# Optimization experiments

Measured on AMD Instinct MI355X. Metric: run time of the kernel, lower is better.

## Reference

```python
import jax, jax.numpy as jnp
import numpy as np

NUM_HEADS = 32
HEAD_DIM = 128
NUM_KV_HEADS = 8
SCALE = 1.0 / np.sqrt(HEAD_DIM)
BATCH = 8
SEQ = 1024
TOTAL = BATCH * SEQ


def setup_inputs() -> dict:
    key = jax.random.key(0)
    kq, kk, kv = jax.random.split(key, 3)
    q = jax.random.normal(kq, (TOTAL, NUM_HEADS * HEAD_DIM), dtype=jnp.float32)
    k = jax.random.normal(kk, (TOTAL, NUM_KV_HEADS * HEAD_DIM), dtype=jnp.float32)
    v = jax.random.normal(kv, (TOTAL, NUM_KV_HEADS * HEAD_DIM), dtype=jnp.float32)
    cu = (jnp.arange(BATCH + 1, dtype=jnp.int32) * SEQ)
    return {"q": q, "k": k, "v": v, "cu_seqlens_q": cu, "cu_seqlens_k": cu}


def reference(q, k, v, cu_seqlens_q, cu_seqlens_k):
    # Prefill path of Attention.forward: causal varlen GQA flash attention.
    # Equal-length sequences -> reshape flat tokens into [B, S, ...].
    B = cu_seqlens_q.shape[0] - 1          # static: number of sequences
    T = q.shape[0]
    S = T // B
    G = NUM_HEADS // NUM_KV_HEADS          # query heads per kv head
    qr = q.reshape(B, S, NUM_KV_HEADS, G, HEAD_DIM)
    kr = k.reshape(B, S, NUM_KV_HEADS, HEAD_DIM)
    vr = v.reshape(B, S, NUM_KV_HEADS, HEAD_DIM)
    # scores: [B, Hkv, G, Sq, Sk]
    scores = jnp.einsum('bqhgd,bkhd->bhgqk', qr, kr) * jnp.float32(SCALE)
    causal = jnp.tril(jnp.ones((S, S), dtype=bool))  # [Sq, Sk]
    scores = jnp.where(causal, scores, jnp.finfo(scores.dtype).min)
    probs = jax.nn.softmax(scores, axis=-1)
    o = jnp.einsum('bhgqk,bkhd->bqhgd', probs, vr)
    return o.reshape(T, NUM_HEADS * HEAD_DIM)
```

## Files before the change

kernel.cpp:

```cpp
#include <hip/hip_runtime.h>
#include <hip/hip_bf16.h>
#include <stdint.h>

typedef __bf16 bf16_t;
typedef __attribute__((ext_vector_type(8))) __bf16 bf16x8;
typedef __attribute__((ext_vector_type(4))) __bf16 bf16x4;
typedef __attribute__((ext_vector_type(4))) float f32x4;

#define NHEADS 32
#define HDIM 128
#define NKV 8
#define GQ 4
#define BATCH 8
#define SEQ 1024
#define TOTAL (BATCH * SEQ)
#define QD (NHEADS * HDIM)
#define KVD (NKV * HDIM)
#define ATT_SCALE 0.08838834764831845f
#define QSCL (0.08838834764831845f * 1.4426950408889634f)

#define QBLK 64
#define KBLK 64
#define NQT (SEQ / QBLK)

__device__ __forceinline__ void gload16(const bf16_t* g, bf16_t* l) {
    __builtin_amdgcn_global_load_lds(
        (const __attribute__((address_space(1))) void*)g,
        (__attribute__((address_space(3))) void*)l,
        16, 0, 0);
}

__global__ __launch_bounds__(256)
void attn_prepass_kernel(const float* __restrict__ kg, const float* __restrict__ vg,
                         bf16_t* __restrict__ kws, bf16_t* __restrict__ vtws)
{
    const int bid = blockIdx.x;
    const int tid = threadIdx.x;
    if (bid < 512) {
        __shared__ bf16_t Lt[128 * 130];
        const int b  = bid >> 6;
        const int hk = (bid >> 3) & 7;
        const int tt = bid & 7;
        const float* vp = vg + ((long)(b * SEQ + tt * 128)) * KVD + hk * HDIM;
        #pragma unroll
        for (int it = 0; it < 16; ++it) {
            int idx = it * 256 + tid;
            int t  = idx >> 5;
            int c4 = (idx & 31) * 4;
            float4 f = *(const float4*)(vp + (long)t * KVD + c4);
            Lt[(c4 + 0) * 130 + t] = (bf16_t)f.x;
            Lt[(c4 + 1) * 130 + t] = (bf16_t)f.y;
            Lt[(c4 + 2) * 130 + t] = (bf16_t)f.z;
            Lt[(c4 + 3) * 130 + t] = (bf16_t)f.w;
        }
        __syncthreads();
        bf16_t* op = vtws + ((long)((b * NKV + hk) * HDIM)) * SEQ + tt * 128;
        #pragma unroll
        for (int jt = 0; jt < 8; ++jt) {
            int jdx = jt * 256 + tid;
            int d  = jdx >> 4;
            int c8 = (jdx & 15) * 8;
            const bf16_t* lp = &Lt[d * 130 + c8];
            uint32_t u0 = *(const uint32_t*)(lp + 0);
            uint32_t u1 = *(const uint32_t*)(lp + 2);
            uint32_t u2 = *(const uint32_t*)(lp + 4);
            uint32_t u3 = *(const uint32_t*)(lp + 6);
            uint4 o; o.x = u0; o.y = u1; o.z = u2; o.w = u3;
            *(uint4*)(op + (long)d * SEQ + c8) = o;
        }
    } else {
        const long total4 = (long)TOTAL * KVD / 4;
        const float4* k4 = (const float4*)kg;
        for (long i = (long)(bid - 512) * 256 + tid; i < total4; i += 1024L * 256) {
            float4 f = k4[i];
            bf16x4 o4;
            o4[0] = (bf16_t)f.x; o4[1] = (bf16_t)f.y;
            o4[2] = (bf16_t)f.z; o4[3] = (bf16_t)f.w;
            *(bf16x4*)(kws + i * 4) = o4;
        }
    }
}

__global__ __launch_bounds__(512, 2)
void attn_fwd_v4(const float* __restrict__ qg, const bf16_t* __restrict__ kws,
                 const bf16_t* __restrict__ vtws, float* __restrict__ og)
{
    __shared__ __align__(16) bf16_t Kl[2][KBLK * HDIM];
    __shared__ __align__(16) bf16_t Vl[2][HDIM * KBLK];
    __shared__ __align__(16) bf16_t Pl[8][16 * 64];

    const int tid  = threadIdx.x;
    const int w    = tid >> 6;
    const int lane = tid & 63;
    const int l4   = lane >> 4;
    const int l16  = lane & 15;

    const int bid = blockIdx.x;
    const int bh  = bid & 63;
    const int pi  = bid >> 6;
    const int b   = bh >> 3;
    const int hk  = bh & 7;
    const int g   = w >> 1;
    const int h   = hk * GQ + g;
    const int rh  = (w & 1) * 32;

    const bf16_t* kbase = kws + (long)(b * SEQ) * KVD + hk * HDIM;
    const bf16_t* vbase = vtws + (long)((b * NKV + hk) * HDIM) * SEQ;
    const int kc0 = w * 2;

    auto issue_tile = [&](int buf, int kt) {
        #pragma unroll
        for (int i = 0; i < 2; ++i) {
            int c = kc0 + i;
            int r = c * 4 + (lane >> 4);
            const bf16_t* gp = kbase + (long)(kt * KBLK + r) * KVD + (((lane & 15) ^ (r & 7)) * 8);
            gload16(gp, &Kl[buf][c * 512]);
        }
        #pragma unroll
        for (int i = 0; i < 2; ++i) {
            int c = kc0 + i;
            int d = c * 8 + (lane >> 3);
            const bf16_t* gp = vbase + (long)d * SEQ + kt * KBLK + (((lane & 7) ^ (d & 7)) * 8);
            gload16(gp, &Vl[buf][c * 512]);
        }
    };

    for (int ph = 0; ph < 2; ++ph) {
        const int qt = ph ? pi : (NQT - 1 - pi);
        const long qtok0 = (long)b * SEQ + qt * QBLK;

        bf16x8 aq[2][4];
        #pragma unroll
        for (int f = 0; f < 2; ++f) {
            const float* qp = qg + (qtok0 + rh + f * 16 + l16) * QD + h * HDIM + l4 * 8;
            #pragma unroll
            for (int s = 0; s < 4; ++s) {
                float4 x = *(const float4*)(qp + s * 32);
                float4 y = *(const float4*)(qp + s * 32 + 4);
                bf16x8 t;
                t[0] = (bf16_t)(x.x * QSCL); t[1] = (bf16_t)(x.y * QSCL);
                t[2] = (bf16_t)(x.z * QSCL); t[3] = (bf16_t)(x.w * QSCL);
                t[4] = (bf16_t)(y.x * QSCL); t[5] = (bf16_t)(y.y * QSCL);
                t[6] = (bf16_t)(y.z * QSCL); t[7] = (bf16_t)(y.w * QSCL);
                aq[f][s] = t;
            }
        }
        __builtin_amdgcn_sched_barrier(0);

        f32x4 accO[2][8];
        f32x4 rsum[2];
        #pragma unroll
        for (int f = 0; f < 2; ++f) {
            #pragma unroll
            for (int n = 0; n < 8; ++n) accO[f][n] = (f32x4){0.f, 0.f, 0.f, 0.f};
            rsum[f] = (f32x4){0.f, 0.f, 0.f, 0.f};
        }

        const int nkt = qt + 1;
        issue_tile(0, 0);
        if (nkt > 1) issue_tile(1, 1);

        for (int kt = 0; kt < nkt; ++kt) {
            const int cur = kt & 1;
            if (kt + 1 < nkt) asm volatile("s_waitcnt vmcnt(4)" ::: "memory");
            else              asm volatile("s_waitcnt vmcnt(0)" ::: "memory");
            __builtin_amdgcn_s_barrier();
            __builtin_amdgcn_sched_barrier(0);

            const bool diag = (kt == qt);
            bf16_t* pw = &Pl[w][0];
            const bf16_t* Kc = &Kl[cur][0];
            const bf16_t* Vc = &Vl[cur][0];

            #pragma unroll
            for (int f = 0; f < 2; ++f) {
                f32x4 accS[4];
                __builtin_amdgcn_s_setprio(1);
                #pragma unroll
                for (int n = 0; n < 4; ++n) {
                    f32x4 acc = (f32x4){0.f, 0.f, 0.f, 0.f};
                    const int r = n * 16 + l16;
                    #pragma unroll
                    for (int s = 0; s < 4; ++s) {
                        int cb = ((s * 64 + l4 * 16) ^ ((r & 7) << 4)) >> 1;
                        bf16x8 bk = *(const bf16x8*)(Kc + r * 128 + cb);
                        acc = __builtin_amdgcn_mfma_f32_16x16x32_bf16(aq[f][s], bk, acc, 0, 0, 0);
                    }
                    accS[n] = acc;
                }
                __builtin_amdgcn_s_setprio(0);

                const int qrow_loc = rh + f * 16 + l4 * 4;
                if (diag) {
                    #pragma unroll
                    for (int n = 0; n < 4; ++n) {
                        #pragma unroll
                        for (int j = 0; j < 4; ++j) {
                            float p = exp2f(accS[n][j]);
                            if (n * 16 + l16 > qrow_loc + j) p = 0.f;
                            accS[n][j] = p;
                            rsum[f][j] += p;
                        }
                    }
                } else {
                    #pragma unroll
                    for (int n = 0; n < 4; ++n) {
                        #pragma unroll
                        for (int j = 0; j < 4; ++j) {
                            float p = exp2f(accS[n][j]);
                            accS[n][j] = p;
                            rsum[f][j] += p;
                        }
                    }
                }

                #pragma unroll
                for (int n = 0; n < 4; ++n) {
                    #pragma unroll
                    for (int j = 0; j < 4; ++j) {
                        int qr = l4 * 4 + j;
                        int cbyte = (n * 32 + l16 * 2) ^ ((qr & 7) << 4);
                        pw[qr * 64 + (cbyte >> 1)] = (bf16_t)accS[n][j];
                    }
                }
                asm volatile("s_waitcnt lgkmcnt(0)" ::: "memory");
                __builtin_amdgcn_sched_barrier(0);
                __builtin_amdgcn_s_setprio(1);
                #pragma unroll
                for (int ks = 0; ks < 2; ++ks) {
                    int cbp = ((ks * 64 + l4 * 16) ^ ((l16 & 7) << 4)) >> 1;
                    bf16x8 ap = *(const bf16x8*)(pw + l16 * 64 + cbp);
                    #pragma unroll
                    for (int n = 0; n < 8; ++n) {
                        int d = n * 16 + l16;
                        int cb = ((ks * 64 + l4 * 16) ^ ((d & 7) << 4)) >> 1;
                        bf16x8 bv = *(const bf16x8*)(Vc + d * 64 + cb);
                        accO[f][n] = __builtin_amdgcn_mfma_f32_16x16x32_bf16(ap, bv, accO[f][n], 0, 0, 0);
                    }
                }
                __builtin_amdgcn_s_setprio(0);
            }
            __builtin_amdgcn_sched_barrier(0);
            __builtin_amdgcn_s_barrier();
            if (kt + 2 < nkt) issue_tile(cur, kt + 2);
        }

        #pragma unroll
        for (int f = 0; f < 2; ++f) {
            #pragma unroll
            for (int j = 0; j < 4; ++j) {
                float r = rsum[f][j];
                r += __shfl_xor(r, 1);
                r += __shfl_xor(r, 2);
                r += __shfl_xor(r, 4);
                r += __shfl_xor(r, 8);
                float inv = 1.f / r;
                float* op = og + (qtok0 + rh + f * 16 + l4 * 4 + j) * QD + h * HDIM;
                #pragma unroll
                for (int n = 0; n < 8; ++n)
                    op[n * 16 + l16] = accO[f][n][j] * inv;
            }
        }
    }
}

#define KPAD 136
#define VPAD 72
#define PPAD 72
__global__ __launch_bounds__(512, 2)
void attn_fwd_v1(const float* __restrict__ qg, const float* __restrict__ kg,
                 const float* __restrict__ vg, float* __restrict__ og)
{
    __shared__ bf16_t Kl[KBLK * KPAD];
    __shared__ bf16_t Vt[HDIM * VPAD];
    __shared__ bf16_t Pl[8 * 16 * PPAD];

    const int tid  = threadIdx.x;
    const int w    = tid >> 6;
    const int lane = tid & 63;
    const int l4   = lane >> 4;
    const int l16  = lane & 15;

    const int bid = blockIdx.x;
    const int bh  = bid % 64;
    const int qt  = (NQT - 1) - bid / 64;
    const int b   = bh / NKV;
    const int hk  = bh % NKV;
    const int g   = w >> 1;
    const int h   = hk * GQ + g;
    const int rh  = (w & 1) * 32;

    const long qtok0 = (long)b * SEQ + qt * QBLK;

    bf16x8 aq[2][4];
    #pragma unroll
    for (int f = 0; f < 2; ++f) {
        const float* qp = qg + (qtok0 + rh + f * 16 + l16) * QD + h * HDIM + l4 * 8;
        #pragma unroll
        for (int s = 0; s < 4; ++s) {
            float4 x = *(const float4*)(qp + s * 32);
            float4 y = *(const float4*)(qp + s * 32 + 4);
            bf16x8 t;
            t[0] = (bf16_t)x.x; t[1] = (bf16_t)x.y; t[2] = (bf16_t)x.z; t[3] = (bf16_t)x.w;
            t[4] = (bf16_t)y.x; t[5] = (bf16_t)y.y; t[6] = (bf16_t)y.z; t[7] = (bf16_t)y.w;
            aq[f][s] = t;
        }
    }

    f32x4 accO[2][8];
    float mrun[2][4], lsum[2][4];
    #pragma unroll
    for (int f = 0; f < 2; ++f) {
        #pragma unroll
        for (int n = 0; n < 8; ++n) accO[f][n] = (f32x4){0.f, 0.f, 0.f, 0.f};
        #pragma unroll
        for (int j = 0; j < 4; ++j) { mrun[f][j] = -1e30f; lsum[f][j] = 0.f; }
    }

    const long ktok0 = (long)b * SEQ;
    const int nkt = qt + 1;

    for (int kt = 0; kt < nkt; ++kt) {
        __syncthreads();
        const float* kp = kg + (ktok0 + kt * KBLK) * KVD + hk * HDIM;
        const float* vp = vg + (ktok0 + kt * KBLK) * KVD + hk * HDIM;
        #pragma unroll
        for (int it = 0; it < 4; ++it) {
            int idx = it * 512 + tid;
            int row = idx >> 5;
            int c4  = (idx & 31) * 4;
            float4 kf = *(const float4*)(kp + (long)row * KVD + c4);
            bf16x4 k4;
            k4[0] = (bf16_t)kf.x; k4[1] = (bf16_t)kf.y; k4[2] = (bf16_t)kf.z; k4[3] = (bf16_t)kf.w;
            *(bf16x4*)(&Kl[row * KPAD + c4]) = k4;
            float4 vf = *(const float4*)(vp + (long)row * KVD + c4);
            const float* vfa = (const float*)&vf;
            #pragma unroll
            for (int m = 0; m < 4; ++m) {
                int d   = c4 + m;
                int blk = (row >> 3) ^ ((d >> 3) & 7);
                Vt[d * VPAD + blk * 8 + (row & 7)] = (bf16_t)vfa[m];
            }
        }
        __syncthreads();

        const bool diag = (kt == qt);
        bf16_t* pw = &Pl[w * 16 * PPAD];

        #pragma unroll
        for (int f = 0; f < 2; ++f) {
            f32x4 accS[4];
            #pragma unroll
            for (int n = 0; n < 4; ++n) {
                f32x4 acc = (f32x4){0.f, 0.f, 0.f, 0.f};
                #pragma unroll
                for (int s = 0; s < 4; ++s) {
                    bf16x8 bk = *(const bf16x8*)(&Kl[(n * 16 + l16) * KPAD + s * 32 + l4 * 8]);
                    acc = __builtin_amdgcn_mfma_f32_16x16x32_bf16(aq[f][s], bk, acc, 0, 0, 0);
                }
                accS[n] = acc;
            }

            const int qrow_loc = rh + f * 16 + l4 * 4;
            float pm[4];
            #pragma unroll
            for (int j = 0; j < 4; ++j) pm[j] = -1e30f;
            #pragma unroll
            for (int n = 0; n < 4; ++n) {
                #pragma unroll
                for (int j = 0; j < 4; ++j) {
                    float sv = accS[n][j] * ATT_SCALE;
                    if (diag && (n * 16 + l16 > qrow_loc + j)) sv = -1e30f;
                    accS[n][j] = sv;
                    pm[j] = fmaxf(pm[j], sv);
                }
            }
            #pragma unroll
            for (int j = 0; j < 4; ++j) {
                float m0 = pm[j];
                m0 = fmaxf(m0, __shfl_xor(m0, 1));
                m0 = fmaxf(m0, __shfl_xor(m0, 2));
                m0 = fmaxf(m0, __shfl_xor(m0, 4));
                m0 = fmaxf(m0, __shfl_xor(m0, 8));
                pm[j] = m0;
            }
            float al[4], rs[4];
            #pragma unroll
            for (int j = 0; j < 4; ++j) {
                float mnew = fmaxf(mrun[f][j], pm[j]);
                al[j] = __expf(mrun[f][j] - mnew);
                mrun[f][j] = mnew;
                rs[j] = 0.f;
            }
            #pragma unroll
            for (int n = 0; n < 4; ++n) {
                #pragma unroll
                for (int j = 0; j < 4; ++j) {
                    float p = __expf(accS[n][j] - mrun[f][j]);
                    accS[n][j] = p;
                    rs[j] += p;
                }
            }
            #pragma unroll
            for (int j = 0; j < 4; ++j) {
                float r = rs[j];
                r += __shfl_xor(r, 1);
                r += __shfl_xor(r, 2);
                r += __shfl_xor(r, 4);
                r += __shfl_xor(r, 8);
                lsum[f][j] = lsum[f][j] * al[j] + r;
            }
            #pragma unroll
            for (int n = 0; n < 8; ++n) {
                #pragma unroll
                for (int j = 0; j < 4; ++j) accO[f][n][j] *= al[j];
            }
            #pragma unroll
            for (int n = 0; n < 4; ++n) {
                #pragma unroll
                for (int j = 0; j < 4; ++j)
                    pw[(l4 * 4 + j) * PPAD + n * 16 + l16] = (bf16_t)accS[n][j];
            }
            asm volatile("s_waitcnt lgkmcnt(0)" ::: "memory");
            __builtin_amdgcn_sched_barrier(0);
            #pragma unroll
            for (int ks = 0; ks < 2; ++ks) {
                bf16x8 ap = *(const bf16x8*)(&pw[l16 * PPAD + ks * 32 + l4 * 8]);
                #pragma unroll
                for (int n = 0; n < 8; ++n) {
                    int d   = n * 16 + l16;
                    int blk = (ks * 4 + l4) ^ ((d >> 3) & 7);
                    bf16x8 bv = *(const bf16x8*)(&Vt[d * VPAD + blk * 8]);
                    accO[f][n] = __builtin_amdgcn_mfma_f32_16x16x32_bf16(ap, bv, accO[f][n], 0, 0, 0);
                }
            }
        }
    }

    #pragma unroll
    for (int f = 0; f < 2; ++f) {
        #pragma unroll
        for (int j = 0; j < 4; ++j) {
            float inv = 1.f / lsum[f][j];
            float* op = og + (qtok0 + rh + f * 16 + l4 * 4 + j) * QD + h * HDIM;
            #pragma unroll
            for (int n = 0; n < 8; ++n)
                op[n * 16 + l16] = accO[f][n][j] * inv;
        }
    }
}

extern "C" void kernel_launch(void* const* d_in, const int* in_sizes, int n_in,
                              void* d_out, int out_size, void* d_ws, size_t ws_size,
                              hipStream_t stream) {
    const float* q = (const float*)d_in[0];
    const float* k = (const float*)d_in[1];
    const float* v = (const float*)d_in[2];
    float* o = (float*)d_out;

    const size_t kws_elems = (size_t)TOTAL * KVD;
    const size_t vws_elems = (size_t)BATCH * NKV * HDIM * SEQ;
    const size_t need = (kws_elems + vws_elems) * sizeof(bf16_t);

    if (ws_size >= need) {
        bf16_t* kws  = (bf16_t*)d_ws;
        bf16_t* vtws = kws + kws_elems;
        attn_prepass_kernel<<<1536, 256, 0, stream>>>(k, v, kws, vtws);
        attn_fwd_v4<<<512, 512, 0, stream>>>(q, kws, vtws, o);
    } else {
        attn_fwd_v1<<<NQT * BATCH * NKV, 512, 0, stream>>>(q, k, v, o);
    }
}
```

Before: 173.6 us.

## Split attention work across 16 waves per block, one 16-row strip each

Raises the attention block from 512 to 1024 threads so each of 16 waves handles one head and one 16-query-row strip instead of two strips. The aim is more waves in flight to hide latency, with fewer registers per wave and each wave loading a single K and V chunk per tile. In exchange the block barriers now synchronize twice as many waves, the P scratch buffer doubles, and launch bounds no longer request two blocks per CU.

```diff
diff --git a/kernel.cpp b/kernel.cpp
--- a/kernel.cpp
+++ b/kernel.cpp
@@ -81,13 +81,13 @@
     }
 }
 
-__global__ __launch_bounds__(512, 2)
-void attn_fwd_v4(const float* __restrict__ qg, const bf16_t* __restrict__ kws,
+__global__ __launch_bounds__(1024)
+void attn_fwd_v5(const float* __restrict__ qg, const bf16_t* __restrict__ kws,
                  const bf16_t* __restrict__ vtws, float* __restrict__ og)
 {
     __shared__ __align__(16) bf16_t Kl[2][KBLK * HDIM];
     __shared__ __align__(16) bf16_t Vl[2][HDIM * KBLK];
-    __shared__ __align__(16) bf16_t Pl[8][16 * 64];
+    __shared__ __align__(16) bf16_t Pl[16][16 * 64];
 
     const int tid  = threadIdx.x;
     const int w    = tid >> 6;
@@ -100,28 +100,23 @@
     const int pi  = bid >> 6;
     const int b   = bh >> 3;
     const int hk  = bh & 7;
-    const int g   = w >> 1;
+    const int g   = w >> 2;
+    const int fs  = w & 3;
     const int h   = hk * GQ + g;
-    const int rh  = (w & 1) * 32;
 
     const bf16_t* kbase = kws + (long)(b * SEQ) * KVD + hk * HDIM;
     const bf16_t* vbase = vtws + (long)((b * NKV + hk) * HDIM) * SEQ;
-    const int kc0 = w * 2;
 
     auto issue_tile = [&](int buf, int kt) {
-        #pragma unroll
-        for (int i = 0; i < 2; ++i) {
-            int c = kc0 + i;
-            int r = c * 4 + (lane >> 4);
+        {
+            int r = w * 4 + (lane >> 4);
             const bf16_t* gp = kbase + (long)(kt * KBLK + r) * KVD + (((lane & 15) ^ (r & 7)) * 8);
-            gload16(gp, &Kl[buf][c * 512]);
-        }
-        #pragma unroll
-        for (int i = 0; i < 2; ++i) {
-            int c = kc0 + i;
-            int d = c * 8 + (lane >> 3);
+            gload16(gp, &Kl[buf][w * 512]);
+        }
+        {
+            int d = w * 8 + (lane >> 3);
             const bf16_t* gp = vbase + (long)d * SEQ + kt * KBLK + (((lane & 7) ^ (d & 7)) * 8);
-            gload16(gp, &Vl[buf][c * 512]);
+            gload16(gp, &Vl[buf][w * 512]);
         }
     };
 
@@ -129,10 +124,9 @@
         const int qt = ph ? pi : (NQT - 1 - pi);
         const long qtok0 = (long)b * SEQ + qt * QBLK;
 
-        bf16x8 aq[2][4];
-        #pragma unroll
-        for (int f = 0; f < 2; ++f) {
-            const float* qp = qg + (qtok0 + rh + f * 16 + l16) * QD + h * HDIM + l4 * 8;
+        bf16x8 aq[4];
+        {
+            const float* qp = qg + (qtok0 + fs * 16 + l16) * QD + h * HDIM + l4 * 8;
             #pragma unroll
             for (int s = 0; s < 4; ++s) {
                 float4 x = *(const float4*)(qp + s * 32);
@@ -142,19 +136,16 @@
                 t[2] = (bf16_t)(x.z * QSCL); t[3] = (bf16_t)(x.w * QSCL);
                 t[4] = (bf16_t)(y.x * QSCL); t[5] = (bf16_t)(y.y * QSCL);
                 t[6] = (bf16_t)(y.z * QSCL); t[7] = (bf16_t)(y.w * QSCL);
-                aq[f][s] = t;
+                aq[s] = t;
             }
         }
         __builtin_amdgcn_sched_barrier(0);
 
-        f32x4 accO[2][8];
-        f32x4 rsum[2];
-        #pragma unroll
-        for (int f = 0; f < 2; ++f) {
-            #pragma unroll
-            for (int n = 0; n < 8; ++n) accO[f][n] = (f32x4){0.f, 0.f, 0.f, 0.f};
-            rsum[f] = (f32x4){0.f, 0.f, 0.f, 0.f};
-        }
+        f32x4 accO[8];
+        f32x4 rsum;
+        #pragma unroll
+        for (int n = 0; n < 8; ++n) accO[n] = (f32x4){0.f, 0.f, 0.f, 0.f};
+        rsum = (f32x4){0.f, 0.f, 0.f, 0.f};
 
         const int nkt = qt + 1;
         issue_tile(0, 0);
@@ -162,7 +153,7 @@
 
         for (int kt = 0; kt < nkt; ++kt) {
             const int cur = kt & 1;
-            if (kt + 1 < nkt) asm volatile("s_waitcnt vmcnt(4)" ::: "memory");
+            if (kt + 1 < nkt) asm volatile("s_waitcnt vmcnt(2)" ::: "memory");
             else              asm volatile("s_waitcnt vmcnt(0)" ::: "memory");
             __builtin_amdgcn_s_barrier();
             __builtin_amdgcn_sched_barrier(0);
@@ -172,94 +163,89 @@
             const bf16_t* Kc = &Kl[cur][0];
             const bf16_t* Vc = &Vl[cur][0];
 
-            #pragma unroll
-            for (int f = 0; f < 2; ++f) {
-                f32x4 accS[4];
-                __builtin_amdgcn_s_setprio(1);
-                #pragma unroll
-                for (int n = 0; n < 4; ++n) {
-                    f32x4 acc = (f32x4){0.f, 0.f, 0.f, 0.f};
-                    const int r = n * 16 + l16;
-                    #pragma unroll
-                    for (int s = 0; s < 4; ++s) {
-                        int cb = ((s * 64 + l4 * 16) ^ ((r & 7) << 4)) >> 1;
-                        bf16x8 bk = *(const bf16x8*)(Kc + r * 128 + cb);
-                        acc = __builtin_amdgcn_mfma_f32_16x16x32_bf16(aq[f][s], bk, acc, 0, 0, 0);
-                    }
-                    accS[n] = acc;
-                }
-                __builtin_amdgcn_s_setprio(0);
-
-                const int qrow_loc = rh + f * 16 + l4 * 4;
-                if (diag) {
-                    #pragma unroll
-                    for (int n = 0; n < 4; ++n) {
-                        #pragma unroll
-                        for (int j = 0; j < 4; ++j) {
-                            float p = exp2f(accS[n][j]);
-                            if (n * 16 + l16 > qrow_loc + j) p = 0.f;
-                            accS[n][j] = p;
-                            rsum[f][j] += p;
-                        }
-                    }
-                } else {
-                    #pragma unroll
-                    for (int n = 0; n < 4; ++n) {
-                        #pragma unroll
-                        for (int j = 0; j < 4; ++j) {
-                            float p = exp2f(accS[n][j]);
-                            accS[n][j] = p;
-                            rsum[f][j] += p;
-                        }
-                    }
-                }
-
+            f32x4 accS[4];
+            __builtin_amdgcn_s_setprio(1);
+            #pragma unroll
+            for (int n = 0; n < 4; ++n) {
+                f32x4 acc = (f32x4){0.f, 0.f, 0.f, 0.f};
+                const int r = n * 16 + l16;
+                #pragma unroll
+                for (int s = 0; s < 4; ++s) {
+                    int cb = ((s * 64 + l4 * 16) ^ ((r & 7) << 4)) >> 1;
+                    bf16x8 bk = *(const bf16x8*)(Kc + r * 128 + cb);
+                    acc = __builtin_amdgcn_mfma_f32_16x16x32_bf16(aq[s], bk, acc, 0, 0, 0);
+                }
+                accS[n] = acc;
+            }
+            __builtin_amdgcn_s_setprio(0);
+
+            const int qrow_loc = fs * 16 + l4 * 4;
+            if (diag) {
                 #pragma unroll
                 for (int n = 0; n < 4; ++n) {
                     #pragma unroll
                     for (int j = 0; j < 4; ++j) {
-                        int qr = l4 * 4 + j;
-                        int cbyte = (n * 32 + l16 * 2) ^ ((qr & 7) << 4);
-                        pw[qr * 64 + (cbyte >> 1)] = (bf16_t)accS[n][j];
+                        float p = exp2f(accS[n][j]);
+                        if (n * 16 + l16 > qrow_loc + j) p = 0.f;
+                        accS[n][j] = p;
+                        rsum[j] += p;
                     }
                 }
-                asm volatile("s_waitcnt lgkmcnt(0)" ::: "memory");
-                __builtin_amdgcn_sched_barrier(0);
-                __builtin_amdgcn_s_setprio(1);
-                #pragma unroll
-                for (int ks = 0; ks < 2; ++ks) {
-                    int cbp = ((ks * 64 + l4 * 16) ^ ((l16 & 7) << 4)) >> 1;
-                    bf16x8 ap = *(const bf16x8*)(pw + l16 * 64 + cbp);
+            } else {
+                #pragma unroll
+                for (int n = 0; n < 4; ++n) {
                     #pragma unroll
-                    for (int n = 0; n < 8; ++n) {
-                        int d = n * 16 + l16;
-                        int cb = ((ks * 64 + l4 * 16) ^ ((d & 7) << 4)) >> 1;
-                        bf16x8 bv = *(const bf16x8*)(Vc + d * 64 + cb);
-                        accO[f][n] = __builtin_amdgcn_mfma_f32_16x16x32_bf16(ap, bv, accO[f][n], 0, 0, 0);
+                    for (int j = 0; j < 4; ++j) {
+                        float p = exp2f(accS[n][j]);
+                        accS[n][j] = p;
+                        rsum[j] += p;
                     }
                 }
-                __builtin_amdgcn_s_setprio(0);
-            }
+            }
+
+            #pragma unroll
+            for (int n = 0; n < 4; ++n) {
+                #pragma unroll
+                for (int j = 0; j < 4; ++j) {
+                    int qr = l4 * 4 + j;
+                    int cbyte = (n * 32 + l16 * 2) ^ ((qr & 7) << 4);
+                    pw[qr * 64 + (cbyte >> 1)] = (bf16_t)accS[n][j];
+                }
+            }
+            asm volatile("s_waitcnt lgkmcnt(0)" ::: "memory");
+            __builtin_amdgcn_sched_barrier(0);
+            __builtin_amdgcn_s_setprio(1);
+            #pragma unroll
+            for (int ks = 0; ks < 2; ++ks) {
+                int cbp = ((ks * 64 + l4 * 16) ^ ((l16 & 7) << 4)) >> 1;
+                bf16x8 ap = *(const bf16x8*)(pw + l16 * 64 + cbp);
+                #pragma unroll
+                for (int n = 0; n < 8; ++n) {
+                    int d = n * 16 + l16;
+                    int cb = ((ks * 64 + l4 * 16) ^ ((d & 7) << 4)) >> 1;
+                    bf16x8 bv = *(const bf16x8*)(Vc + d * 64 + cb);
+                    accO[n] = __builtin_amdgcn_mfma_f32_16x16x32_bf16(ap, bv, accO[n], 0, 0, 0);
+                }
+            }
+            __builtin_amdgcn_s_setprio(0);
+
             __builtin_amdgcn_sched_barrier(0);
             __builtin_amdgcn_s_barrier();
             if (kt + 2 < nkt) issue_tile(cur, kt + 2);
         }
 
         #pragma unroll
-        for (int f = 0; f < 2; ++f) {
-            #pragma unroll
-            for (int j = 0; j < 4; ++j) {
-                float r = rsum[f][j];
-                r += __shfl_xor(r, 1);
-                r += __shfl_xor(r, 2);
-                r += __shfl_xor(r, 4);
-                r += __shfl_xor(r, 8);
-                float inv = 1.f / r;
-                float* op = og + (qtok0 + rh + f * 16 + l4 * 4 + j) * QD + h * HDIM;
-                #pragma unroll
-                for (int n = 0; n < 8; ++n)
-                    op[n * 16 + l16] = accO[f][n][j] * inv;
-            }
+        for (int j = 0; j < 4; ++j) {
+            float r = rsum[j];
+            r += __shfl_xor(r, 1);
+            r += __shfl_xor(r, 2);
+            r += __shfl_xor(r, 4);
+            r += __shfl_xor(r, 8);
+            float inv = 1.f / r;
+            float* op = og + (qtok0 + fs * 16 + l4 * 4 + j) * QD + h * HDIM;
+            #pragma unroll
+            for (int n = 0; n < 8; ++n)
+                op[n * 16 + l16] = accO[n][j] * inv;
         }
     }
 }
@@ -466,7 +452,7 @@
         bf16_t* kws  = (bf16_t*)d_ws;
         bf16_t* vtws = kws + kws_elems;
         attn_prepass_kernel<<<1536, 256, 0, stream>>>(k, v, kws, vtws);
-        attn_fwd_v4<<<512, 512, 0, stream>>>(q, kws, vtws, o);
+        attn_fwd_v5<<<512, 1024, 0, stream>>>(q, kws, vtws, o);
     } else {
         attn_fwd_v1<<<NQT * BATCH * NKV, 512, 0, stream>>>(q, k, v, o);
     }
```

Result: slower. 178.3 us (+2.7%).

## Switch attention inner loops to 32x32x16 MFMA tiles with diagonal-half skip

Applied to the files above, without the earlier changes.

Rewrites the per-wave QK^T and PV computation to use 32x32x16 bf16 MFMA instructions over a full 32-row query slice instead of two 16-row passes of 16x16x32 MFMAs. This cuts LDS operand reads per FLOP and the instruction count, and the P staging buffer grows to 32x64 per wave. On the diagonal tile, waves owning the upper 32 query rows skip the second key half entirely, since it is fully masked. The trade-off is larger accumulator register tiles (16 floats each), which may pressure registers at 2 blocks per CU.

```diff
diff --git a/kernel.cpp b/kernel.cpp
--- a/kernel.cpp
+++ b/kernel.cpp
@@ -6,6 +6,7 @@
 typedef __attribute__((ext_vector_type(8))) __bf16 bf16x8;
 typedef __attribute__((ext_vector_type(4))) __bf16 bf16x4;
 typedef __attribute__((ext_vector_type(4))) float f32x4;
+typedef __attribute__((ext_vector_type(16))) float f32x16;
 
 #define NHEADS 32
 #define HDIM 128
@@ -28,6 +29,13 @@
         (const __attribute__((address_space(1))) void*)g,
         (__attribute__((address_space(3))) void*)l,
         16, 0, 0);
+}
+
+__device__ __forceinline__ f32x16 zero16() {
+    f32x16 z;
+    #pragma unroll
+    for (int j = 0; j < 16; ++j) z[j] = 0.f;
+    return z;
 }
 
 __global__ __launch_bounds__(256)
@@ -82,18 +90,18 @@
 }
 
 __global__ __launch_bounds__(512, 2)
-void attn_fwd_v4(const float* __restrict__ qg, const bf16_t* __restrict__ kws,
+void attn_fwd_v6(const float* __restrict__ qg, const bf16_t* __restrict__ kws,
                  const bf16_t* __restrict__ vtws, float* __restrict__ og)
 {
     __shared__ __align__(16) bf16_t Kl[2][KBLK * HDIM];
     __shared__ __align__(16) bf16_t Vl[2][HDIM * KBLK];
-    __shared__ __align__(16) bf16_t Pl[8][16 * 64];
+    __shared__ __align__(16) bf16_t Pl[8][32 * 64];
 
     const int tid  = threadIdx.x;
     const int w    = tid >> 6;
     const int lane = tid & 63;
-    const int l4   = lane >> 4;
-    const int l16  = lane & 15;
+    const int l31  = lane & 31;
+    const int l2   = lane >> 5;
 
     const int bid = blockIdx.x;
     const int bh  = bid & 63;
@@ -101,8 +109,9 @@
     const int b   = bh >> 3;
     const int hk  = bh & 7;
     const int g   = w >> 1;
+    const int half = w & 1;
+    const int rh  = half * 32;
     const int h   = hk * GQ + g;
-    const int rh  = (w & 1) * 32;
 
     const bf16_t* kbase = kws + (long)(b * SEQ) * KVD + hk * HDIM;
     const bf16_t* vbase = vtws + (long)((b * NKV + hk) * HDIM) * SEQ;
@@ -129,32 +138,29 @@
         const int qt = ph ? pi : (NQT - 1 - pi);
         const long qtok0 = (long)b * SEQ + qt * QBLK;
 
-        bf16x8 aq[2][4];
-        #pragma unroll
-        for (int f = 0; f < 2; ++f) {
-            const float* qp = qg + (qtok0 + rh + f * 16 + l16) * QD + h * HDIM + l4 * 8;
-            #pragma unroll
-            for (int s = 0; s < 4; ++s) {
-                float4 x = *(const float4*)(qp + s * 32);
-                float4 y = *(const float4*)(qp + s * 32 + 4);
+        bf16x8 aq[8];
+        {
+            const float* qp = qg + (qtok0 + rh + l31) * QD + h * HDIM + l2 * 8;
+            #pragma unroll
+            for (int s = 0; s < 8; ++s) {
+                float4 x = *(const float4*)(qp + s * 16);
+                float4 y = *(const float4*)(qp + s * 16 + 4);
                 bf16x8 t;
                 t[0] = (bf16_t)(x.x * QSCL); t[1] = (bf16_t)(x.y * QSCL);
                 t[2] = (bf16_t)(x.z * QSCL); t[3] = (bf16_t)(x.w * QSCL);
                 t[4] = (bf16_t)(y.x * QSCL); t[5] = (bf16_t)(y.y * QSCL);
                 t[6] = (bf16_t)(y.z * QSCL); t[7] = (bf16_t)(y.w * QSCL);
-                aq[f][s] = t;
+                aq[s] = t;
             }
         }
         __builtin_amdgcn_sched_barrier(0);
 
-        f32x4 accO[2][8];
-        f32x4 rsum[2];
-        #pragma unroll
-        for (int f = 0; f < 2; ++f) {
-            #pragma unroll
-            for (int n = 0; n < 8; ++n) accO[f][n] = (f32x4){0.f, 0.f, 0.f, 0.f};
-            rsum[f] = (f32x4){0.f, 0.f, 0.f, 0.f};
-        }
+        f32x16 accO[4];
+        #pragma unroll
+        for (int n = 0; n < 4; ++n) accO[n] = zero16();
+        float rsum[16];
+        #pragma unroll
+        for (int r = 0; r < 16; ++r) rsum[r] = 0.f;
 
         const int nkt = qt + 1;
         issue_tile(0, 0);
@@ -167,99 +173,107 @@
             __builtin_amdgcn_s_barrier();
             __builtin_amdgcn_sched_barrier(0);
 
-            const bool diag = (kt == qt);
+            const bool diag  = (kt == qt);
+            const bool skip1 = diag && (rh == 0);
             bf16_t* pw = &Pl[w][0];
             const bf16_t* Kc = &Kl[cur][0];
             const bf16_t* Vc = &Vl[cur][0];
 
-            #pragma unroll
-            for (int f = 0; f < 2; ++f) {
-                f32x4 accS[4];
-                __builtin_amdgcn_s_setprio(1);
-                #pragma unroll
-                for (int n = 0; n < 4; ++n) {
-                    f32x4 acc = (f32x4){0.f, 0.f, 0.f, 0.f};
-                    const int r = n * 16 + l16;
-                    #pragma unroll
-                    for (int s = 0; s < 4; ++s) {
-                        int cb = ((s * 64 + l4 * 16) ^ ((r & 7) << 4)) >> 1;
-                        bf16x8 bk = *(const bf16x8*)(Kc + r * 128 + cb);
-                        acc = __builtin_amdgcn_mfma_f32_16x16x32_bf16(aq[f][s], bk, acc, 0, 0, 0);
-                    }
-                    accS[n] = acc;
-                }
-                __builtin_amdgcn_s_setprio(0);
-
-                const int qrow_loc = rh + f * 16 + l4 * 4;
-                if (diag) {
-                    #pragma unroll
-                    for (int n = 0; n < 4; ++n) {
-                        #pragma unroll
-                        for (int j = 0; j < 4; ++j) {
-                            float p = exp2f(accS[n][j]);
-                            if (n * 16 + l16 > qrow_loc + j) p = 0.f;
-                            accS[n][j] = p;
-                            rsum[f][j] += p;
-                        }
-                    }
-                } else {
-                    #pragma unroll
-                    for (int n = 0; n < 4; ++n) {
-                        #pragma unroll
-                        for (int j = 0; j < 4; ++j) {
-                            float p = exp2f(accS[n][j]);
-                            accS[n][j] = p;
-                            rsum[f][j] += p;
-                        }
-                    }
-                }
-
-                #pragma unroll
-                for (int n = 0; n < 4; ++n) {
-                    #pragma unroll
-                    for (int j = 0; j < 4; ++j) {
-                        int qr = l4 * 4 + j;
-                        int cbyte = (n * 32 + l16 * 2) ^ ((qr & 7) << 4);
-                        pw[qr * 64 + (cbyte >> 1)] = (bf16_t)accS[n][j];
-                    }
-                }
-                asm volatile("s_waitcnt lgkmcnt(0)" ::: "memory");
-                __builtin_amdgcn_sched_barrier(0);
-                __builtin_amdgcn_s_setprio(1);
-                #pragma unroll
-                for (int ks = 0; ks < 2; ++ks) {
-                    int cbp = ((ks * 64 + l4 * 16) ^ ((l16 & 7) << 4)) >> 1;
-                    bf16x8 ap = *(const bf16x8*)(pw + l16 * 64 + cbp);
-                    #pragma unroll
-                    for (int n = 0; n < 8; ++n) {
-                        int d = n * 16 + l16;
-                        int cb = ((ks * 64 + l4 * 16) ^ ((d & 7) << 4)) >> 1;
-                        bf16x8 bv = *(const bf16x8*)(Vc + d * 64 + cb);
-                        accO[f][n] = __builtin_amdgcn_mfma_f32_16x16x32_bf16(ap, bv, accO[f][n], 0, 0, 0);
-                    }
-                }
-                __builtin_amdgcn_s_setprio(0);
-            }
+            f32x16 accS[2];
+            __builtin_amdgcn_s_setprio(1);
+            {
+                f32x16 acc = zero16();
+                #pragma unroll
+                for (int s = 0; s < 8; ++s) {
+                    int elem = (s * 16 + l2 * 8) ^ ((l31 & 7) << 3);
+                    bf16x8 bk = *(const bf16x8*)(Kc + l31 * 128 + elem);
+                    acc = __builtin_amdgcn_mfma_f32_32x32x16_bf16(aq[s], bk, acc, 0, 0, 0);
+                }
+                accS[0] = acc;
+            }
+            if (!skip1) {
+                f32x16 acc = zero16();
+                #pragma unroll
+                for (int s = 0; s < 8; ++s) {
+                    int elem = (s * 16 + l2 * 8) ^ ((l31 & 7) << 3);
+                    bf16x8 bk = *(const bf16x8*)(Kc + (32 + l31) * 128 + elem);
+                    acc = __builtin_amdgcn_mfma_f32_32x32x16_bf16(aq[s], bk, acc, 0, 0, 0);
+                }
+                accS[1] = acc;
+            } else {
+                accS[1] = zero16();
+            }
+            __builtin_amdgcn_s_setprio(0);
+
+            const int qb = rh + 4 * l2;
+            #pragma unroll
+            for (int r = 0; r < 16; ++r) {
+                const int rowoff = (r & 3) + 8 * (r >> 2);
+                float p = exp2f(accS[0][r]);
+                if (diag && (l31 > qb + rowoff)) p = 0.f;
+                accS[0][r] = p;
+                rsum[r] += p;
+            }
+            if (!skip1) {
+                #pragma unroll
+                for (int r = 0; r < 16; ++r) {
+                    const int rowoff = (r & 3) + 8 * (r >> 2);
+                    float p = exp2f(accS[1][r]);
+                    if (diag && (32 + l31 > qb + rowoff)) p = 0.f;
+                    accS[1][r] = p;
+                    rsum[r] += p;
+                }
+            }
+
+            #pragma unroll
+            for (int n = 0; n < 2; ++n) {
+                #pragma unroll
+                for (int r = 0; r < 16; ++r) {
+                    const int row = (r & 3) + 8 * (r >> 2) + 4 * l2;
+                    const int col = n * 32 + l31;
+                    pw[row * 64 + (col ^ ((row & 7) << 3))] = (bf16_t)accS[n][r];
+                }
+            }
+            asm volatile("s_waitcnt lgkmcnt(0)" ::: "memory");
+            __builtin_amdgcn_sched_barrier(0);
+
+            __builtin_amdgcn_s_setprio(1);
+            bf16x8 pa[4];
+            #pragma unroll
+            for (int ks = 0; ks < 4; ++ks) {
+                int elem = (ks * 16 + l2 * 8) ^ ((l31 & 7) << 3);
+                pa[ks] = *(const bf16x8*)(pw + l31 * 64 + elem);
+            }
+            #pragma unroll
+            for (int n = 0; n < 4; ++n) {
+                #pragma unroll
+                for (int ks = 0; ks < 4; ++ks) {
+                    int elem = (ks * 16 + l2 * 8) ^ ((l31 & 7) << 3);
+                    bf16x8 bv = *(const bf16x8*)(Vc + (n * 32 + l31) * 64 + elem);
+                    accO[n] = __builtin_amdgcn_mfma_f32_32x32x16_bf16(pa[ks], bv, accO[n], 0, 0, 0);
+                }
+            }
+            __builtin_amdgcn_s_setprio(0);
+
             __builtin_amdgcn_sched_barrier(0);
             __builtin_amdgcn_s_barrier();
             if (kt + 2 < nkt) issue_tile(cur, kt + 2);
         }
 
         #pragma unroll
-        for (int f = 0; f < 2; ++f) {
-            #pragma unroll
-            for (int j = 0; j < 4; ++j) {
-                float r = rsum[f][j];
-                r += __shfl_xor(r, 1);
-                r += __shfl_xor(r, 2);
-                r += __shfl_xor(r, 4);
-                r += __shfl_xor(r, 8);
-                float inv = 1.f / r;
-                float* op = og + (qtok0 + rh + f * 16 + l4 * 4 + j) * QD + h * HDIM;
-                #pragma unroll
-                for (int n = 0; n < 8; ++n)
-                    op[n * 16 + l16] = accO[f][n][j] * inv;
-            }
+        for (int r = 0; r < 16; ++r) {
+            const int rowoff = (r & 3) + 8 * (r >> 2);
+            float s = rsum[r];
+            s += __shfl_xor(s, 1);
+            s += __shfl_xor(s, 2);
+            s += __shfl_xor(s, 4);
+            s += __shfl_xor(s, 8);
+            s += __shfl_xor(s, 16);
+            float inv = 1.f / s;
+            float* op = og + (qtok0 + rh + rowoff + 4 * l2) * QD + h * HDIM + l31;
+            #pragma unroll
+            for (int n = 0; n < 4; ++n)
+                op[n * 32] = accO[n][r] * inv;
         }
     }
 }
@@ -466,7 +480,7 @@
         bf16_t* kws  = (bf16_t*)d_ws;
         bf16_t* vtws = kws + kws_elems;
         attn_prepass_kernel<<<1536, 256, 0, stream>>>(k, v, kws, vtws);
-        attn_fwd_v4<<<512, 512, 0, stream>>>(q, kws, vtws, o);
+        attn_fwd_v6<<<512, 512, 0, stream>>>(q, kws, vtws, o);
     } else {
         attn_fwd_v1<<<NQT * BATCH * NKV, 512, 0, stream>>>(q, k, v, o);
     }
```

After: 175.5 us. No clear change (+1.1%).
